# Kernel tuning notes

Hardware: AMD Instinct MI355X
Metric: run time of the kernel (lower is better)

Reference implementation:

```python
import jax, jax.numpy as jnp
import numpy as np

B, L, D, KSIZE = 16, 2048, 128, 8  # batch, seq_len, d_model (=input=hidden), window size


def setup_inputs() -> dict:
    key = jax.random.key(0)
    ks = jax.random.split(key, 5)
    s = 1.0 / np.sqrt(D)  # PyTorch RNN init range
    return {
        "x": jax.random.normal(ks[0], (B, L, D), jnp.float32),
        "W_ih": jax.random.uniform(ks[1], (3 * D, D), jnp.float32, -s, s),
        "W_hh": jax.random.uniform(ks[2], (3 * D, D), jnp.float32, -s, s),
        "b_ih": jax.random.uniform(ks[3], (3 * D,), jnp.float32, -s, s),
        "b_hh": jax.random.uniform(ks[4], (3 * D,), jnp.float32, -s, s),
    }


def _local_gru(x, W_ih, W_hh, b_ih, b_hh, ksize):
    # x: [B, L, D]. Equivalent to get_K (left zero-pad + sliding windows of
    # length ksize) followed by a GRU over each window, keeping the last
    # hidden state. Instead of materializing [B*L, ksize, D] windows, we scan
    # over the ksize window positions: at step t, every window reads the
    # shifted sequence x_pad[:, t:t+L, :].
    Bb, Ll, Dd = x.shape
    H = W_hh.shape[1]
    pad = jnp.zeros((Bb, ksize - 1, Dd), x.dtype)
    xp = jnp.concatenate([pad, x], axis=1)  # [B, L+k-1, D]
    xs = jnp.stack([xp[:, t:t + Ll, :] for t in range(ksize)], axis=0)  # [k, B, L, D]

    Wir, Wiz, Win = jnp.split(W_ih, 3, axis=0)
    Whr, Whz, Whn = jnp.split(W_hh, 3, axis=0)
    bir, biz, bin_ = jnp.split(b_ih, 3)
    bhr, bhz, bhn = jnp.split(b_hh, 3)

    def step(h, xt):  # h, xt: [B, L, H/D]
        r = jax.nn.sigmoid(xt @ Wir.T + bir + h @ Whr.T + bhr)
        z = jax.nn.sigmoid(xt @ Wiz.T + biz + h @ Whz.T + bhz)
        n = jnp.tanh(xt @ Win.T + bin_ + r * (h @ Whn.T + bhn))
        h = (1.0 - z) * n + z * h
        return h, None

    h0 = jnp.zeros((Bb, Ll, H), x.dtype)
    h_last, _ = jax.lax.scan(step, h0, xs)
    return h_last  # [B, L, H]: last hidden state of each length-ksize window


def reference(x, W_ih, W_hh, b_ih, b_hh):
    return _local_gru(x, W_ih, W_hh, b_ih, b_hh, KSIZE)
```

## Files before the change

### kernel.cpp

```cpp
#include <hip/hip_runtime.h>
#include <hip/hip_bf16.h>

#define DEV __device__ __forceinline__

typedef __attribute__((ext_vector_type(8))) short bf16x8;
typedef __attribute__((ext_vector_type(4))) float f32x4;

constexpr int Bq = 16, Lq = 2048, Dq = 128, KW = 8;
constexpr int G3 = 3 * Dq;
constexpr float L2E = 1.4426950408889634f;

DEV float exp2f_hw(float x) { return __builtin_amdgcn_exp2f(x); }

DEV unsigned short f2bf(float f) {
    union { __hip_bfloat16 h; unsigned short u; } v;
    v.h = __float2bfloat16(f);
    return v.u;
}
DEV float bf2f(unsigned short s) { return __uint_as_float(((unsigned)s) << 16); }

DEV float sigm2(float y) { return __builtin_amdgcn_rcpf(1.f + exp2f_hw(-y)); }
DEV float tanh2(float y) {
    float e = exp2f_hw(y);
    return fmaf(-2.f, __builtin_amdgcn_rcpf(e + 1.f), 1.f);
}

DEV bf16x8 pack8s(float4 a, float4 b, float s) {
    bf16x8 r;
    r[0] = (short)f2bf(a.x * s); r[1] = (short)f2bf(a.y * s);
    r[2] = (short)f2bf(a.z * s); r[3] = (short)f2bf(a.w * s);
    r[4] = (short)f2bf(b.x * s); r[5] = (short)f2bf(b.y * s);
    r[6] = (short)f2bf(b.z * s); r[7] = (short)f2bf(b.w * s);
    return r;
}
DEV int2 packbf4(float a, float b, float c, float d) {
    int2 r;
    r.x = (int)(((unsigned)f2bf(b) << 16) | (unsigned)f2bf(a));
    r.y = (int)(((unsigned)f2bf(d) << 16) | (unsigned)f2bf(c));
    return r;
}

__global__ __launch_bounds__(512, 2) void k_proj(
    const float* __restrict__ x, const float* __restrict__ W_ih,
    const float* __restrict__ b_ih, const float* __restrict__ b_hh,
    unsigned short* __restrict__ Xp)
{
    __shared__ __attribute__((aligned(16))) unsigned char lds[64 * 768];

    const int tid = threadIdx.x;
    const int lane = tid & 63, w = tid >> 6;
    const int l15 = lane & 15, l4 = lane >> 4;
    const int r0 = blockIdx.x * 64;

#pragma unroll
    for (int it = 0; it < 4; ++it) {
        int c = it * 512 + tid;
        int byte = c << 4;
        int row = byte >> 9;
        int wb = byte & 511;
        float4 v = *(const float4*)((const char*)(x + (size_t)r0 * Dq) + byte);
        int dst = row * 256 + ((wb >> 1) ^ ((row & 7) << 4));
        *(int2*)(lds + dst) = packbf4(v.x, v.y, v.z, v.w);
    }

    bf16x8 afr[3][4];
#pragma unroll
    for (int mt = 0; mt < 3; ++mt)
#pragma unroll
        for (int kc = 0; kc < 4; ++kc) {
            int row = 48 * w + 16 * mt + l15;
            int k0 = 32 * kc + 8 * l4;
            const float* p = W_ih + row * Dq + k0;
            afr[mt][kc] = pack8s(*(const float4*)p, *(const float4*)(p + 4), 1.f);
        }
    float fs[3], bias[3][4];
#pragma unroll
    for (int mt = 0; mt < 3; ++mt) {
        int rbase = 48 * w + 16 * mt + 4 * l4;
        fs[mt] = (rbase < 2 * Dq) ? L2E : 2.f * L2E;
#pragma unroll
        for (int r = 0; r < 4; ++r) {
            int row = rbase + r;
            float bv = b_ih[row] + (row < 2 * Dq ? b_hh[row] : 0.f);
            bias[mt][r] = bv * fs[mt];
        }
    }
    __syncthreads();

    f32x4 acc[3][4];
#pragma unroll
    for (int mt = 0; mt < 3; ++mt)
#pragma unroll
        for (int nt = 0; nt < 4; ++nt) {
            acc[mt][nt][0] = 0.f; acc[mt][nt][1] = 0.f;
            acc[mt][nt][2] = 0.f; acc[mt][nt][3] = 0.f;
        }

#pragma unroll
    for (int kc = 0; kc < 4; ++kc) {
        bf16x8 bfr[4];
#pragma unroll
        for (int nt = 0; nt < 4; ++nt) {
            int row = 16 * nt + l15;
            int off = row * 256 + ((64 * kc + 16 * l4) ^ ((row & 7) << 4));
            bfr[nt] = *(const bf16x8*)(lds + off);
        }
#pragma unroll
        for (int nt = 0; nt < 4; ++nt)
#pragma unroll
            for (int mt = 0; mt < 3; ++mt)
                acc[mt][nt] = __builtin_amdgcn_mfma_f32_16x16x32_bf16(
                    afr[mt][kc], bfr[nt], acc[mt][nt], 0, 0, 0);
    }

    __syncthreads();

#pragma unroll
    for (int mt = 0; mt < 3; ++mt)
#pragma unroll
        for (int nt = 0; nt < 4; ++nt) {
            int r = 16 * nt + l15;
            int g = 48 * w + 16 * mt + 4 * l4;
            int sw = ((r + 7) & 7) << 3;
            int2 pk = packbf4(fmaf(acc[mt][nt][0], fs[mt], bias[mt][0]),
                              fmaf(acc[mt][nt][1], fs[mt], bias[mt][1]),
                              fmaf(acc[mt][nt][2], fs[mt], bias[mt][2]),
                              fmaf(acc[mt][nt][3], fs[mt], bias[mt][3]));
            *(int2*)(lds + 2 * (size_t)(r * G3 + (g ^ sw))) = pk;
        }
    __syncthreads();

    {
        int4* dst = (int4*)(Xp + (size_t)r0 * G3);
#pragma unroll
        for (int it = 0; it < 6; ++it)
            dst[it * 512 + tid] = ((const int4*)lds)[it * 512 + tid];
    }
}

__global__ __launch_bounds__(512, 2) void k_rnn(
    const unsigned short* __restrict__ Xp, const float* __restrict__ W_hh,
    const float* __restrict__ b_ih, const float* __restrict__ b_hh,
    float* __restrict__ out)
{
    __shared__ __attribute__((aligned(16))) unsigned char xpt[71 * 768];
    __shared__ __attribute__((aligned(16))) unsigned char hls[64 * 256];

    const int tid = threadIdx.x;
    const int lane = tid & 63, w = tid >> 6;
    const int l15 = lane & 15, l4 = lane >> 4;
    const int b = blockIdx.x >> 5;
    const int l0 = (blockIdx.x & 31) << 6;

    bf16x8 afr[3][4];
#pragma unroll
    for (int g = 0; g < 3; ++g) {
        float fg = (g < 2) ? L2E : 2.f * L2E;
#pragma unroll
        for (int kc = 0; kc < 4; ++kc) {
            int row = 128 * g + 16 * w + l15;
            int k0 = 32 * kc + 8 * l4;
            const float* p = W_hh + row * Dq + k0;
            afr[g][kc] = pack8s(*(const float4*)p, *(const float4*)(p + 4), fg);
        }
    }
    const int u0 = 16 * w + 4 * l4;
    f32x4 bhn4;
#pragma unroll
    for (int r = 0; r < 4; ++r) bhn4[r] = b_hh[2 * Dq + u0 + r] * (2.f * L2E);

    if (l0 == 0) {
        for (int i = tid; i < 7 * G3; i += 512) {
            int tr = i / G3, g = i - tr * G3;
            float fg = (g < 2 * Dq) ? L2E : 2.f * L2E;
            float v = (b_ih[g] + (g < 2 * Dq ? b_hh[g] : 0.f)) * fg;
            ((unsigned short*)xpt)[tr * G3 + (g ^ ((tr & 7) << 3))] = f2bf(v);
        }
        const int4* src = (const int4*)(Xp + (size_t)b * Lq * G3);
#pragma unroll
        for (int it = 0; it < 6; ++it)
            ((int4*)(xpt + 7 * 768))[it * 512 + tid] = src[it * 512 + tid];
    } else {
        const int4* src = (const int4*)(Xp + ((size_t)b * Lq + l0 - 7) * G3);
        for (int c = tid; c < 71 * 48; c += 512)
            ((int4*)xpt)[c] = src[c];
    }
    __syncthreads();

    f32x4 h[4];

#pragma unroll
    for (int nt = 0; nt < 4; ++nt) {
        int tr = 16 * nt + l15;
        int base = tr * G3;
        int s = (tr & 7) << 3;
        const ushort4 qr = *(const ushort4*)(xpt + 2 * (size_t)(base + ((0 * Dq + u0) ^ s)));
        const ushort4 qz = *(const ushort4*)(xpt + 2 * (size_t)(base + ((1 * Dq + u0) ^ s)));
        const ushort4 qn = *(const ushort4*)(xpt + 2 * (size_t)(base + ((2 * Dq + u0) ^ s)));
        float xr[4] = {bf2f(qr.x), bf2f(qr.y), bf2f(qr.z), bf2f(qr.w)};
        float xz[4] = {bf2f(qz.x), bf2f(qz.y), bf2f(qz.z), bf2f(qz.w)};
        float xn[4] = {bf2f(qn.x), bf2f(qn.y), bf2f(qn.z), bf2f(qn.w)};
#pragma unroll
        for (int r = 0; r < 4; ++r) {
            float rv = sigm2(xr[r]);
            float zv = sigm2(xz[r]);
            float nv = tanh2(fmaf(rv, bhn4[r], xn[r]));
            h[nt][r] = nv - zv * nv;
        }
    }
#pragma unroll
    for (int nt = 0; nt < 4; ++nt) {
        int win = 16 * nt + l15;
        int off = win * 256 + ((2 * u0) ^ ((win & 7) << 4));
        *(int2*)(hls + off) = packbf4(h[nt][0], h[nt][1], h[nt][2], h[nt][3]);
    }
    __syncthreads();

    for (int t = 1; t < 8; ++t) {
        f32x4 ar[4], az[4], an[4];
#pragma unroll
        for (int nt = 0; nt < 4; ++nt) {
            ar[nt][0] = 0.f; ar[nt][1] = 0.f; ar[nt][2] = 0.f; ar[nt][3] = 0.f;
            az[nt] = ar[nt];
            an[nt] = bhn4;
        }
#pragma unroll
        for (int kc = 0; kc < 4; ++kc) {
            bf16x8 bfr[4];
#pragma unroll
            for (int nt = 0; nt < 4; ++nt) {
                int row = 16 * nt + l15;
                int off = row * 256 + ((64 * kc + 16 * l4) ^ ((row & 7) << 4));
                bfr[nt] = *(const bf16x8*)(hls + off);
            }
#pragma unroll
            for (int nt = 0; nt < 4; ++nt) {
                ar[nt] = __builtin_amdgcn_mfma_f32_16x16x32_bf16(afr[0][kc], bfr[nt], ar[nt], 0, 0, 0);
                az[nt] = __builtin_amdgcn_mfma_f32_16x16x32_bf16(afr[1][kc], bfr[nt], az[nt], 0, 0, 0);
                an[nt] = __builtin_amdgcn_mfma_f32_16x16x32_bf16(afr[2][kc], bfr[nt], an[nt], 0, 0, 0);
            }
        }
#pragma unroll
        for (int nt = 0; nt < 4; ++nt) {
            int tr = 16 * nt + l15 + t;
            int base = tr * G3;
            int s = (tr & 7) << 3;
            const ushort4 qr = *(const ushort4*)(xpt + 2 * (size_t)(base + ((0 * Dq + u0) ^ s)));
            const ushort4 qz = *(const ushort4*)(xpt + 2 * (size_t)(base + ((1 * Dq + u0) ^ s)));
            const ushort4 qn = *(const ushort4*)(xpt + 2 * (size_t)(base + ((2 * Dq + u0) ^ s)));
            float xr[4] = {bf2f(qr.x), bf2f(qr.y), bf2f(qr.z), bf2f(qr.w)};
            float xz[4] = {bf2f(qz.x), bf2f(qz.y), bf2f(qz.z), bf2f(qz.w)};
            float xn[4] = {bf2f(qn.x), bf2f(qn.y), bf2f(qn.z), bf2f(qn.w)};
#pragma unroll
            for (int r = 0; r < 4; ++r) {
                float rv = sigm2(ar[nt][r] + xr[r]);
                float zv = sigm2(az[nt][r] + xz[r]);
                float nv = tanh2(fmaf(rv, an[nt][r], xn[r]));
                h[nt][r] = nv + zv * (h[nt][r] - nv);
            }
        }
        if (t < 7) {
            __syncthreads();
#pragma unroll
            for (int nt = 0; nt < 4; ++nt) {
                int win = 16 * nt + l15;
                int off = win * 256 + ((2 * u0) ^ ((win & 7) << 4));
                *(int2*)(hls + off) = packbf4(h[nt][0], h[nt][1], h[nt][2], h[nt][3]);
            }
            __syncthreads();
        }
    }

#pragma unroll
    for (int nt = 0; nt < 4; ++nt) {
        size_t idx = ((size_t)(b * Lq + l0 + 16 * nt + l15)) * Dq + u0;
        *(f32x4*)(out + idx) = h[nt];
    }
}

extern "C" void kernel_launch(void* const* d_in, const int* in_sizes, int n_in,
                              void* d_out, int out_size, void* d_ws, size_t ws_size,
                              hipStream_t stream) {
    const float* x    = (const float*)d_in[0];
    const float* W_ih = (const float*)d_in[1];
    const float* W_hh = (const float*)d_in[2];
    const float* b_ih = (const float*)d_in[3];
    const float* b_hh = (const float*)d_in[4];
    float* out = (float*)d_out;
    unsigned short* Xp = (unsigned short*)d_ws;

    k_proj<<<dim3(512), dim3(512), 0, stream>>>(x, W_ih, b_ih, b_hh, Xp);
    k_rnn<<<dim3(512), dim3(512), 0, stream>>>(Xp, W_hh, b_ih, b_hh, out);
}
```

Measured before the change: 144.7 us.

## Split projection buffer into rz/n parts and double-buffer hidden state

The projection kernel now writes the r/z gate projections and the n gate projections to separate workspace buffers. The recurrent kernel stages only the r/z part in shared memory and reads the n projections straight from global memory, issuing those loads early so they overlap the MFMA work. The r/z input projections are used as the initial MFMA accumulator values, which removes separate adds. The hidden-state tile is double-buffered so each step needs one barrier instead of two. The trade-off is extra global-load latency inside the recurrence and extra padding-row handling for the n gate.

After: 141.3 us. 2.3% less time.

```diff
diff --git a/kernel.cpp b/kernel.cpp
--- a/kernel.cpp
+++ b/kernel.cpp
@@ -6,7 +6,8 @@
 typedef __attribute__((ext_vector_type(8))) short bf16x8;
 typedef __attribute__((ext_vector_type(4))) float f32x4;
 
-constexpr int Bq = 16, Lq = 2048, Dq = 128, KW = 8;
+constexpr int Bq = 16, Lq = 2048, Dq = 128;
+constexpr int RZ = 2 * Dq;
 constexpr int G3 = 3 * Dq;
 constexpr float L2E = 1.4426950408889634f;
 
@@ -43,7 +44,7 @@
 __global__ __launch_bounds__(512, 2) void k_proj(
     const float* __restrict__ x, const float* __restrict__ W_ih,
     const float* __restrict__ b_ih, const float* __restrict__ b_hh,
-    unsigned short* __restrict__ Xp)
+    unsigned short* __restrict__ Xp_rz, unsigned short* __restrict__ Xp_n)
 {
     __shared__ __attribute__((aligned(16))) unsigned char lds[64 * 768];
 
@@ -77,11 +78,11 @@
 #pragma unroll
     for (int mt = 0; mt < 3; ++mt) {
         int rbase = 48 * w + 16 * mt + 4 * l4;
-        fs[mt] = (rbase < 2 * Dq) ? L2E : 2.f * L2E;
+        fs[mt] = (rbase < RZ) ? L2E : 2.f * L2E;
 #pragma unroll
         for (int r = 0; r < 4; ++r) {
             int row = rbase + r;
-            float bv = b_ih[row] + (row < 2 * Dq ? b_hh[row] : 0.f);
+            float bv = b_ih[row] + (row < RZ ? b_hh[row] : 0.f);
             bias[mt][r] = bv * fs[mt];
         }
     }
@@ -126,25 +127,35 @@
                               fmaf(acc[mt][nt][1], fs[mt], bias[mt][1]),
                               fmaf(acc[mt][nt][2], fs[mt], bias[mt][2]),
                               fmaf(acc[mt][nt][3], fs[mt], bias[mt][3]));
-            *(int2*)(lds + 2 * (size_t)(r * G3 + (g ^ sw))) = pk;
+            if (48 * w + 16 * mt < RZ) {
+                *(int2*)(lds + r * 512 + ((g ^ sw) << 1)) = pk;
+            } else {
+                int u = g - RZ;
+                *(int2*)(lds + 32768 + r * 256 + ((u ^ sw) << 1)) = pk;
+            }
         }
     __syncthreads();
 
     {
-        int4* dst = (int4*)(Xp + (size_t)r0 * G3);
-#pragma unroll
-        for (int it = 0; it < 6; ++it)
+        int4* dst = (int4*)(Xp_rz + (size_t)r0 * RZ);
+#pragma unroll
+        for (int it = 0; it < 4; ++it)
             dst[it * 512 + tid] = ((const int4*)lds)[it * 512 + tid];
+        int4* dstn = (int4*)(Xp_n + (size_t)r0 * Dq);
+        const int4* srcn = (const int4*)(lds + 32768);
+#pragma unroll
+        for (int it = 0; it < 2; ++it)
+            dstn[it * 512 + tid] = srcn[it * 512 + tid];
     }
 }
 
 __global__ __launch_bounds__(512, 2) void k_rnn(
-    const unsigned short* __restrict__ Xp, const float* __restrict__ W_hh,
-    const float* __restrict__ b_ih, const float* __restrict__ b_hh,
-    float* __restrict__ out)
+    const unsigned short* __restrict__ Xp_rz, const unsigned short* __restrict__ Xp_n,
+    const float* __restrict__ W_hh, const float* __restrict__ b_ih,
+    const float* __restrict__ b_hh, float* __restrict__ out)
 {
-    __shared__ __attribute__((aligned(16))) unsigned char xpt[71 * 768];
-    __shared__ __attribute__((aligned(16))) unsigned char hls[64 * 256];
+    __shared__ __attribute__((aligned(16))) unsigned char xpt[71 * 512];
+    __shared__ __attribute__((aligned(16))) unsigned char hls[2 * 64 * 256];
 
     const int tid = threadIdx.x;
     const int lane = tid & 63, w = tid >> 6;
@@ -165,24 +176,26 @@
         }
     }
     const int u0 = 16 * w + 4 * l4;
-    f32x4 bhn4;
-#pragma unroll
-    for (int r = 0; r < 4; ++r) bhn4[r] = b_hh[2 * Dq + u0 + r] * (2.f * L2E);
+    f32x4 bhn4, bn4;
+#pragma unroll
+    for (int r = 0; r < 4; ++r) {
+        bhn4[r] = b_hh[RZ + u0 + r] * (2.f * L2E);
+        bn4[r]  = b_ih[RZ + u0 + r] * (2.f * L2E);
+    }
 
     if (l0 == 0) {
-        for (int i = tid; i < 7 * G3; i += 512) {
-            int tr = i / G3, g = i - tr * G3;
-            float fg = (g < 2 * Dq) ? L2E : 2.f * L2E;
-            float v = (b_ih[g] + (g < 2 * Dq ? b_hh[g] : 0.f)) * fg;
-            ((unsigned short*)xpt)[tr * G3 + (g ^ ((tr & 7) << 3))] = f2bf(v);
-        }
-        const int4* src = (const int4*)(Xp + (size_t)b * Lq * G3);
-#pragma unroll
-        for (int it = 0; it < 6; ++it)
-            ((int4*)(xpt + 7 * 768))[it * 512 + tid] = src[it * 512 + tid];
+        for (int i = tid; i < 7 * RZ; i += 512) {
+            int tr = i >> 8, g = i & 255;
+            float v = (b_ih[g] + b_hh[g]) * L2E;
+            ((unsigned short*)xpt)[tr * RZ + (g ^ ((tr & 7) << 3))] = f2bf(v);
+        }
+        const int4* src = (const int4*)(Xp_rz + (size_t)b * Lq * RZ);
+#pragma unroll
+        for (int it = 0; it < 4; ++it)
+            ((int4*)(xpt + 7 * 512))[it * 512 + tid] = src[it * 512 + tid];
     } else {
-        const int4* src = (const int4*)(Xp + ((size_t)b * Lq + l0 - 7) * G3);
-        for (int c = tid; c < 71 * 48; c += 512)
+        const int4* src = (const int4*)(Xp_rz + ((size_t)b * Lq + l0 - 7) * RZ);
+        for (int c = tid; c < 71 * 32; c += 512)
             ((int4*)xpt)[c] = src[c];
     }
     __syncthreads();
@@ -192,19 +205,21 @@
 #pragma unroll
     for (int nt = 0; nt < 4; ++nt) {
         int tr = 16 * nt + l15;
-        int base = tr * G3;
         int s = (tr & 7) << 3;
-        const ushort4 qr = *(const ushort4*)(xpt + 2 * (size_t)(base + ((0 * Dq + u0) ^ s)));
-        const ushort4 qz = *(const ushort4*)(xpt + 2 * (size_t)(base + ((1 * Dq + u0) ^ s)));
-        const ushort4 qn = *(const ushort4*)(xpt + 2 * (size_t)(base + ((2 * Dq + u0) ^ s)));
+        int ln = l0 + tr - 7;
+        int lnc = ln < 0 ? 0 : ln;
+        const ushort4 qn = *(const ushort4*)(Xp_n + (size_t)(b * Lq + lnc) * Dq + (u0 ^ s));
+        const ushort4 qr = *(const ushort4*)(xpt + ((tr * RZ + (u0 ^ s)) << 1));
+        const ushort4 qz = *(const ushort4*)(xpt + ((tr * RZ + ((Dq + u0) ^ s)) << 1));
         float xr[4] = {bf2f(qr.x), bf2f(qr.y), bf2f(qr.z), bf2f(qr.w)};
         float xz[4] = {bf2f(qz.x), bf2f(qz.y), bf2f(qz.z), bf2f(qz.w)};
         float xn[4] = {bf2f(qn.x), bf2f(qn.y), bf2f(qn.z), bf2f(qn.w)};
 #pragma unroll
         for (int r = 0; r < 4; ++r) {
+            float xnv = ln < 0 ? bn4[r] : xn[r];
             float rv = sigm2(xr[r]);
             float zv = sigm2(xz[r]);
-            float nv = tanh2(fmaf(rv, bhn4[r], xn[r]));
+            float nv = tanh2(fmaf(rv, bhn4[r], xnv));
             h[nt][r] = nv - zv * nv;
         }
     }
@@ -217,11 +232,26 @@
     __syncthreads();
 
     for (int t = 1; t < 8; ++t) {
+        const int rdo = ((t - 1) & 1) << 14;
+        const int wro = (t & 1) << 14;
+
         f32x4 ar[4], az[4], an[4];
-#pragma unroll
-        for (int nt = 0; nt < 4; ++nt) {
-            ar[nt][0] = 0.f; ar[nt][1] = 0.f; ar[nt][2] = 0.f; ar[nt][3] = 0.f;
-            az[nt] = ar[nt];
+        ushort4 qn_s[4];
+        int ln_s[4];
+#pragma unroll
+        for (int nt = 0; nt < 4; ++nt) {
+            int tr = 16 * nt + l15 + t;
+            int s = (tr & 7) << 3;
+            int ln = l0 + tr - 7;
+            int lnc = ln < 0 ? 0 : ln;
+            ln_s[nt] = ln;
+            qn_s[nt] = *(const ushort4*)(Xp_n + (size_t)(b * Lq + lnc) * Dq + (u0 ^ s));
+            const ushort4 qr = *(const ushort4*)(xpt + ((tr * RZ + (u0 ^ s)) << 1));
+            const ushort4 qz = *(const ushort4*)(xpt + ((tr * RZ + ((Dq + u0) ^ s)) << 1));
+            ar[nt][0] = bf2f(qr.x); ar[nt][1] = bf2f(qr.y);
+            ar[nt][2] = bf2f(qr.z); ar[nt][3] = bf2f(qr.w);
+            az[nt][0] = bf2f(qz.x); az[nt][1] = bf2f(qz.y);
+            az[nt][2] = bf2f(qz.z); az[nt][3] = bf2f(qz.w);
             an[nt] = bhn4;
         }
 #pragma unroll
@@ -230,7 +260,7 @@
 #pragma unroll
             for (int nt = 0; nt < 4; ++nt) {
                 int row = 16 * nt + l15;
-                int off = row * 256 + ((64 * kc + 16 * l4) ^ ((row & 7) << 4));
+                int off = rdo + row * 256 + ((64 * kc + 16 * l4) ^ ((row & 7) << 4));
                 bfr[nt] = *(const bf16x8*)(hls + off);
             }
 #pragma unroll
@@ -242,29 +272,22 @@
         }
 #pragma unroll
         for (int nt = 0; nt < 4; ++nt) {
-            int tr = 16 * nt + l15 + t;
-            int base = tr * G3;
-            int s = (tr & 7) << 3;
-            const ushort4 qr = *(const ushort4*)(xpt + 2 * (size_t)(base + ((0 * Dq + u0) ^ s)));
-            const ushort4 qz = *(const ushort4*)(xpt + 2 * (size_t)(base + ((1 * Dq + u0) ^ s)));
-            const ushort4 qn = *(const ushort4*)(xpt + 2 * (size_t)(base + ((2 * Dq + u0) ^ s)));
-            float xr[4] = {bf2f(qr.x), bf2f(qr.y), bf2f(qr.z), bf2f(qr.w)};
-            float xz[4] = {bf2f(qz.x), bf2f(qz.y), bf2f(qz.z), bf2f(qz.w)};
-            float xn[4] = {bf2f(qn.x), bf2f(qn.y), bf2f(qn.z), bf2f(qn.w)};
+            float xn[4] = {bf2f(qn_s[nt].x), bf2f(qn_s[nt].y),
+                           bf2f(qn_s[nt].z), bf2f(qn_s[nt].w)};
 #pragma unroll
             for (int r = 0; r < 4; ++r) {
-                float rv = sigm2(ar[nt][r] + xr[r]);
-                float zv = sigm2(az[nt][r] + xz[r]);
-                float nv = tanh2(fmaf(rv, an[nt][r], xn[r]));
+                float xnv = ln_s[nt] < 0 ? bn4[r] : xn[r];
+                float rv = sigm2(ar[nt][r]);
+                float zv = sigm2(az[nt][r]);
+                float nv = tanh2(fmaf(rv, an[nt][r], xnv));
                 h[nt][r] = nv + zv * (h[nt][r] - nv);
             }
         }
         if (t < 7) {
-            __syncthreads();
 #pragma unroll
             for (int nt = 0; nt < 4; ++nt) {
                 int win = 16 * nt + l15;
-                int off = win * 256 + ((2 * u0) ^ ((win & 7) << 4));
+                int off = wro + win * 256 + ((2 * u0) ^ ((win & 7) << 4));
                 *(int2*)(hls + off) = packbf4(h[nt][0], h[nt][1], h[nt][2], h[nt][3]);
             }
             __syncthreads();
@@ -287,8 +310,9 @@
     const float* b_ih = (const float*)d_in[3];
     const float* b_hh = (const float*)d_in[4];
     float* out = (float*)d_out;
-    unsigned short* Xp = (unsigned short*)d_ws;
-
-    k_proj<<<dim3(512), dim3(512), 0, stream>>>(x, W_ih, b_ih, b_hh, Xp);
-    k_rnn<<<dim3(512), dim3(512), 0, stream>>>(Xp, W_hh, b_ih, b_hh, out);
-}
+    unsigned short* Xp_rz = (unsigned short*)d_ws;
+    unsigned short* Xp_n  = Xp_rz + (size_t)Bq * Lq * RZ;
+
+    k_proj<<<dim3(512), dim3(512), 0, stream>>>(x, W_ih, b_ih, b_hh, Xp_rz, Xp_n);
+    k_rnn<<<dim3(512), dim3(512), 0, stream>>>(Xp_rz, Xp_n, W_hh, b_ih, b_hh, out);
+}
```

## Transpose projection workspace and read gate inputs directly from global in RNN kernel

Applied to the files above, without the earlier changes.

The projection kernel now writes its output in a gate-group-major layout (groups of 4 units × sequence positions), so the recurrent kernel can load each lane's r/z/n inputs as 8-byte global reads instead of staging a 71-row tile in LDS. The RNN kernel drops that tile, halves the windows per block (32 instead of 64) and doubles the grid to 1024 blocks. It double-buffers the hidden-state LDS so only one barrier is needed per step, and it prefetches the next step's inputs before the MFMAs. Padding at sequence start is handled with precomputed bias values. In exchange, each of the 8 steps now issues global loads and more blocks must reload W_hh.

Result: slower. 156.6 us (+8.3%).

```diff
diff --git a/kernel.cpp b/kernel.cpp
--- a/kernel.cpp
+++ b/kernel.cpp
@@ -6,8 +6,8 @@
 typedef __attribute__((ext_vector_type(8))) short bf16x8;
 typedef __attribute__((ext_vector_type(4))) float f32x4;
 
-constexpr int Bq = 16, Lq = 2048, Dq = 128, KW = 8;
-constexpr int G3 = 3 * Dq;
+constexpr int Bq = 16, Lq = 2048, Dq = 128;
+constexpr int RZ = 2 * Dq;
 constexpr float L2E = 1.4426950408889634f;
 
 DEV float exp2f_hw(float x) { return __builtin_amdgcn_exp2f(x); }
@@ -17,7 +17,8 @@
     v.h = __float2bfloat16(f);
     return v.u;
 }
-DEV float bf2f(unsigned short s) { return __uint_as_float(((unsigned)s) << 16); }
+DEV float bfu_lo(int u) { return __uint_as_float((unsigned)u << 16); }
+DEV float bfu_hi(int u) { return __uint_as_float((unsigned)u & 0xffff0000u); }
 
 DEV float sigm2(float y) { return __builtin_amdgcn_rcpf(1.f + exp2f_hw(-y)); }
 DEV float tanh2(float y) {
@@ -43,9 +44,9 @@
 __global__ __launch_bounds__(512, 2) void k_proj(
     const float* __restrict__ x, const float* __restrict__ W_ih,
     const float* __restrict__ b_ih, const float* __restrict__ b_hh,
-    unsigned short* __restrict__ Xp)
+    unsigned short* __restrict__ XpT)
 {
-    __shared__ __attribute__((aligned(16))) unsigned char lds[64 * 768];
+    __shared__ __attribute__((aligned(16))) unsigned char lds[96 * 64 * 8];
 
     const int tid = threadIdx.x;
     const int lane = tid & 63, w = tid >> 6;
@@ -77,11 +78,11 @@
 #pragma unroll
     for (int mt = 0; mt < 3; ++mt) {
         int rbase = 48 * w + 16 * mt + 4 * l4;
-        fs[mt] = (rbase < 2 * Dq) ? L2E : 2.f * L2E;
+        fs[mt] = (rbase < RZ) ? L2E : 2.f * L2E;
 #pragma unroll
         for (int r = 0; r < 4; ++r) {
             int row = rbase + r;
-            float bv = b_ih[row] + (row < 2 * Dq ? b_hh[row] : 0.f);
+            float bv = b_ih[row] + (row < RZ ? b_hh[row] : 0.f);
             bias[mt][r] = bv * fs[mt];
         }
     }
@@ -120,37 +121,40 @@
 #pragma unroll
         for (int nt = 0; nt < 4; ++nt) {
             int r = 16 * nt + l15;
-            int g = 48 * w + 16 * mt + 4 * l4;
-            int sw = ((r + 7) & 7) << 3;
+            int g4 = 12 * w + 4 * mt + l4;
             int2 pk = packbf4(fmaf(acc[mt][nt][0], fs[mt], bias[mt][0]),
                               fmaf(acc[mt][nt][1], fs[mt], bias[mt][1]),
                               fmaf(acc[mt][nt][2], fs[mt], bias[mt][2]),
                               fmaf(acc[mt][nt][3], fs[mt], bias[mt][3]));
-            *(int2*)(lds + 2 * (size_t)(r * G3 + (g ^ sw))) = pk;
+            *(int2*)(lds + (((g4 << 6) + r) << 3)) = pk;
         }
     __syncthreads();
 
     {
-        int4* dst = (int4*)(Xp + (size_t)r0 * G3);
-#pragma unroll
-        for (int it = 0; it < 6; ++it)
-            dst[it * 512 + tid] = ((const int4*)lds)[it * 512 + tid];
+        const int lr0 = r0 & 2047;
+        const int bb = r0 >> 11;
+#pragma unroll
+        for (int it = 0; it < 6; ++it) {
+            int idx = it * 512 + tid;
+            int g4 = idx >> 5, off = idx & 31;
+            size_t d = (((size_t)(bb * 96 + g4) << 11) + lr0) >> 1;
+            ((int4*)XpT)[d + off] = ((const int4*)lds)[idx];
+        }
     }
 }
 
 __global__ __launch_bounds__(512, 2) void k_rnn(
-    const unsigned short* __restrict__ Xp, const float* __restrict__ W_hh,
+    const int2* __restrict__ Xp2, const float* __restrict__ W_hh,
     const float* __restrict__ b_ih, const float* __restrict__ b_hh,
     float* __restrict__ out)
 {
-    __shared__ __attribute__((aligned(16))) unsigned char xpt[71 * 768];
-    __shared__ __attribute__((aligned(16))) unsigned char hls[64 * 256];
+    __shared__ __attribute__((aligned(16))) unsigned char hls[2 * 32 * 256];
 
     const int tid = threadIdx.x;
     const int lane = tid & 63, w = tid >> 6;
     const int l15 = lane & 15, l4 = lane >> 4;
-    const int b = blockIdx.x >> 5;
-    const int l0 = (blockIdx.x & 31) << 6;
+    const int b = blockIdx.x >> 6;
+    const int l0 = (blockIdx.x & 63) << 5;
 
     bf16x8 afr[3][4];
 #pragma unroll
@@ -165,41 +169,46 @@
         }
     }
     const int u0 = 16 * w + 4 * l4;
+    const float4 bir = *(const float4*)(b_ih + u0);
+    const float4 bhr = *(const float4*)(b_hh + u0);
+    const float4 biz = *(const float4*)(b_ih + Dq + u0);
+    const float4 bhz = *(const float4*)(b_hh + Dq + u0);
+    const float4 bin_ = *(const float4*)(b_ih + RZ + u0);
+    const float4 bhn = *(const float4*)(b_hh + RZ + u0);
     f32x4 bhn4;
-#pragma unroll
-    for (int r = 0; r < 4; ++r) bhn4[r] = b_hh[2 * Dq + u0 + r] * (2.f * L2E);
-
-    if (l0 == 0) {
-        for (int i = tid; i < 7 * G3; i += 512) {
-            int tr = i / G3, g = i - tr * G3;
-            float fg = (g < 2 * Dq) ? L2E : 2.f * L2E;
-            float v = (b_ih[g] + (g < 2 * Dq ? b_hh[g] : 0.f)) * fg;
-            ((unsigned short*)xpt)[tr * G3 + (g ^ ((tr & 7) << 3))] = f2bf(v);
-        }
-        const int4* src = (const int4*)(Xp + (size_t)b * Lq * G3);
-#pragma unroll
-        for (int it = 0; it < 6; ++it)
-            ((int4*)(xpt + 7 * 768))[it * 512 + tid] = src[it * 512 + tid];
-    } else {
-        const int4* src = (const int4*)(Xp + ((size_t)b * Lq + l0 - 7) * G3);
-        for (int c = tid; c < 71 * 48; c += 512)
-            ((int4*)xpt)[c] = src[c];
-    }
-    __syncthreads();
-
-    f32x4 h[4];
-
-#pragma unroll
-    for (int nt = 0; nt < 4; ++nt) {
-        int tr = 16 * nt + l15;
-        int base = tr * G3;
-        int s = (tr & 7) << 3;
-        const ushort4 qr = *(const ushort4*)(xpt + 2 * (size_t)(base + ((0 * Dq + u0) ^ s)));
-        const ushort4 qz = *(const ushort4*)(xpt + 2 * (size_t)(base + ((1 * Dq + u0) ^ s)));
-        const ushort4 qn = *(const ushort4*)(xpt + 2 * (size_t)(base + ((2 * Dq + u0) ^ s)));
-        float xr[4] = {bf2f(qr.x), bf2f(qr.y), bf2f(qr.z), bf2f(qr.w)};
-        float xz[4] = {bf2f(qz.x), bf2f(qz.y), bf2f(qz.z), bf2f(qz.w)};
-        float xn[4] = {bf2f(qn.x), bf2f(qn.y), bf2f(qn.z), bf2f(qn.w)};
+    bhn4[0] = bhn.x * (2.f * L2E); bhn4[1] = bhn.y * (2.f * L2E);
+    bhn4[2] = bhn.z * (2.f * L2E); bhn4[3] = bhn.w * (2.f * L2E);
+    const int2 pbr = packbf4((bir.x + bhr.x) * L2E, (bir.y + bhr.y) * L2E,
+                             (bir.z + bhr.z) * L2E, (bir.w + bhr.w) * L2E);
+    const int2 pbz = packbf4((biz.x + bhz.x) * L2E, (biz.y + bhz.y) * L2E,
+                             (biz.z + bhz.z) * L2E, (biz.w + bhz.w) * L2E);
+    const int2 pbn = packbf4(bin_.x * (2.f * L2E), bin_.y * (2.f * L2E),
+                             bin_.z * (2.f * L2E), bin_.w * (2.f * L2E));
+
+    const size_t rowr = ((size_t)(b * 96) + (u0 >> 2)) << 11;
+    const int2* pr = Xp2 + rowr + (l0 + l15 - 7);
+    const int2* pz = pr + (size_t)32 * 2048;
+    const int2* pn = pr + (size_t)64 * 2048;
+    const bool edge = (l0 == 0);
+
+    f32x4 h[2];
+
+#pragma unroll
+    for (int nt = 0; nt < 2; ++nt) {
+        int2 qr, qz, qn;
+        if (!edge) {
+            qr = pr[16 * nt]; qz = pz[16 * nt]; qn = pn[16 * nt];
+        } else {
+            int ln = 16 * nt + l15 - 7;
+            int lnc = ln < 0 ? 0 : ln;
+            qr = (Xp2 + rowr)[lnc];
+            qz = (Xp2 + rowr + (size_t)32 * 2048)[lnc];
+            qn = (Xp2 + rowr + (size_t)64 * 2048)[lnc];
+            if (ln < 0) { qr = pbr; qz = pbz; qn = pbn; }
+        }
+        float xr[4] = {bfu_lo(qr.x), bfu_hi(qr.x), bfu_lo(qr.y), bfu_hi(qr.y)};
+        float xz[4] = {bfu_lo(qz.x), bfu_hi(qz.x), bfu_lo(qz.y), bfu_hi(qz.y)};
+        float xn[4] = {bfu_lo(qn.x), bfu_hi(qn.x), bfu_lo(qn.y), bfu_hi(qn.y)};
 #pragma unroll
         for (int r = 0; r < 4; ++r) {
             float rv = sigm2(xr[r]);
@@ -209,7 +218,7 @@
         }
     }
 #pragma unroll
-    for (int nt = 0; nt < 4; ++nt) {
+    for (int nt = 0; nt < 2; ++nt) {
         int win = 16 * nt + l15;
         int off = win * 256 + ((2 * u0) ^ ((win & 7) << 4));
         *(int2*)(hls + off) = packbf4(h[nt][0], h[nt][1], h[nt][2], h[nt][3]);
@@ -217,40 +226,59 @@
     __syncthreads();
 
     for (int t = 1; t < 8; ++t) {
-        f32x4 ar[4], az[4], an[4];
-#pragma unroll
-        for (int nt = 0; nt < 4; ++nt) {
+        int2 qr_s[2], qz_s[2], qn_s[2];
+        if (!edge) {
+#pragma unroll
+            for (int nt = 0; nt < 2; ++nt) {
+                qr_s[nt] = pr[16 * nt + t];
+                qz_s[nt] = pz[16 * nt + t];
+                qn_s[nt] = pn[16 * nt + t];
+            }
+        } else {
+#pragma unroll
+            for (int nt = 0; nt < 2; ++nt) {
+                int ln = 16 * nt + l15 + t - 7;
+                int lnc = ln < 0 ? 0 : ln;
+                qr_s[nt] = (Xp2 + rowr)[lnc];
+                qz_s[nt] = (Xp2 + rowr + (size_t)32 * 2048)[lnc];
+                qn_s[nt] = (Xp2 + rowr + (size_t)64 * 2048)[lnc];
+                if (ln < 0) { qr_s[nt] = pbr; qz_s[nt] = pbz; qn_s[nt] = pbn; }
+            }
+        }
+
+        const int rdo = ((t - 1) & 1) << 13;
+        const int wro = (t & 1) << 13;
+        f32x4 ar[2], az[2], an[2];
+#pragma unroll
+        for (int nt = 0; nt < 2; ++nt) {
             ar[nt][0] = 0.f; ar[nt][1] = 0.f; ar[nt][2] = 0.f; ar[nt][3] = 0.f;
             az[nt] = ar[nt];
             an[nt] = bhn4;
         }
 #pragma unroll
         for (int kc = 0; kc < 4; ++kc) {
-            bf16x8 bfr[4];
-#pragma unroll
-            for (int nt = 0; nt < 4; ++nt) {
-                int row = 16 * nt + l15;
-                int off = row * 256 + ((64 * kc + 16 * l4) ^ ((row & 7) << 4));
+            bf16x8 bfr[2];
+#pragma unroll
+            for (int nt = 0; nt < 2; ++nt) {
+                int win = 16 * nt + l15;
+                int off = rdo + win * 256 + ((64 * kc + 16 * l4) ^ ((win & 7) << 4));
                 bfr[nt] = *(const bf16x8*)(hls + off);
             }
 #pragma unroll
-            for (int nt = 0; nt < 4; ++nt) {
+            for (int nt = 0; nt < 2; ++nt) {
                 ar[nt] = __builtin_amdgcn_mfma_f32_16x16x32_bf16(afr[0][kc], bfr[nt], ar[nt], 0, 0, 0);
                 az[nt] = __builtin_amdgcn_mfma_f32_16x16x32_bf16(afr[1][kc], bfr[nt], az[nt], 0, 0, 0);
                 an[nt] = __builtin_amdgcn_mfma_f32_16x16x32_bf16(afr[2][kc], bfr[nt], an[nt], 0, 0, 0);
             }
         }
 #pragma unroll
-        for (int nt = 0; nt < 4; ++nt) {
-            int tr = 16 * nt + l15 + t;
-            int base = tr * G3;
-            int s = (tr & 7) << 3;
-            const ushort4 qr = *(const ushort4*)(xpt + 2 * (size_t)(base + ((0 * Dq + u0) ^ s)));
-            const ushort4 qz = *(const ushort4*)(xpt + 2 * (size_t)(base + ((1 * Dq + u0) ^ s)));
-            const ushort4 qn = *(const ushort4*)(xpt + 2 * (size_t)(base + ((2 * Dq + u0) ^ s)));
-            float xr[4] = {bf2f(qr.x), bf2f(qr.y), bf2f(qr.z), bf2f(qr.w)};
-            float xz[4] = {bf2f(qz.x), bf2f(qz.y), bf2f(qz.z), bf2f(qz.w)};
-            float xn[4] = {bf2f(qn.x), bf2f(qn.y), bf2f(qn.z), bf2f(qn.w)};
+        for (int nt = 0; nt < 2; ++nt) {
+            float xr[4] = {bfu_lo(qr_s[nt].x), bfu_hi(qr_s[nt].x),
+                           bfu_lo(qr_s[nt].y), bfu_hi(qr_s[nt].y)};
+            float xz[4] = {bfu_lo(qz_s[nt].x), bfu_hi(qz_s[nt].x),
+                           bfu_lo(qz_s[nt].y), bfu_hi(qz_s[nt].y)};
+            float xn[4] = {bfu_lo(qn_s[nt].x), bfu_hi(qn_s[nt].x),
+                           bfu_lo(qn_s[nt].y), bfu_hi(qn_s[nt].y)};
 #pragma unroll
             for (int r = 0; r < 4; ++r) {
                 float rv = sigm2(ar[nt][r] + xr[r]);
@@ -260,19 +288,18 @@
             }
         }
         if (t < 7) {
+#pragma unroll
+            for (int nt = 0; nt < 2; ++nt) {
+                int win = 16 * nt + l15;
+                int off = wro + win * 256 + ((2 * u0) ^ ((win & 7) << 4));
+                *(int2*)(hls + off) = packbf4(h[nt][0], h[nt][1], h[nt][2], h[nt][3]);
+            }
             __syncthreads();
-#pragma unroll
-            for (int nt = 0; nt < 4; ++nt) {
-                int win = 16 * nt + l15;
-                int off = win * 256 + ((2 * u0) ^ ((win & 7) << 4));
-                *(int2*)(hls + off) = packbf4(h[nt][0], h[nt][1], h[nt][2], h[nt][3]);
-            }
-            __syncthreads();
-        }
-    }
-
-#pragma unroll
-    for (int nt = 0; nt < 4; ++nt) {
+        }
+    }
+
+#pragma unroll
+    for (int nt = 0; nt < 2; ++nt) {
         size_t idx = ((size_t)(b * Lq + l0 + 16 * nt + l15)) * Dq + u0;
         *(f32x4*)(out + idx) = h[nt];
     }
@@ -287,8 +314,8 @@
     const float* b_ih = (const float*)d_in[3];
     const float* b_hh = (const float*)d_in[4];
     float* out = (float*)d_out;
-    unsigned short* Xp = (unsigned short*)d_ws;
-
-    k_proj<<<dim3(512), dim3(512), 0, stream>>>(x, W_ih, b_ih, b_hh, Xp);
-    k_rnn<<<dim3(512), dim3(512), 0, stream>>>(Xp, W_hh, b_ih, b_hh, out);
-}
+    unsigned short* XpT = (unsigned short*)d_ws;
+
+    k_proj<<<dim3(512), dim3(512), 0, stream>>>(x, W_ih, b_ih, b_hh, XpT);
+    k_rnn<<<dim3(1024), dim3(512), 0, stream>>>((const int2*)XpT, W_hh, b_ih, b_hh, out);
+}
```
